# Optimization experiments

Hardware: AMD Instinct MI355X
Metric: run time of the kernel (lower is better)

The kernel has to match this reference:

```python
import jax, jax.numpy as jnp
import numpy as np

D_IN = 128
HID = 32
HEADS = 8
OUT = 16
N = 50000
E = 400000
NEG_SLOPE = 0.2


def setup_inputs() -> dict:
    key = jax.random.key(0)
    ks = jax.random.split(key, 12)
    s = lambda k, sh: jax.random.normal(k, sh, dtype=jnp.float32) * 0.05
    return {
        "x": jax.random.normal(ks[0], (N, D_IN), dtype=jnp.float32),
        "edge_index": jax.random.randint(ks[1], (2, E), 0, N, dtype=jnp.int64),
        # conv_1: GATv2, heads=8, concat=True
        "W1l": s(ks[2], (D_IN, HEADS * HID)),
        "W1r": s(ks[3], (D_IN, HEADS * HID)),
        "att1": s(ks[4], (HEADS, HID)),
        "b1": jnp.zeros((HEADS * HID,), dtype=jnp.float32),
        # conv_2: GATv2, heads=1, concat=False
        "W2l": s(ks[5], (HEADS * HID, HID)),
        "W2r": s(ks[6], (HEADS * HID, HID)),
        "att2": s(ks[7], (1, HID)),
        "b2": jnp.zeros((HID,), dtype=jnp.float32),
        # final linear
        "Wlin": s(ks[8], (HID, OUT)),
        "blin": jnp.zeros((OUT,), dtype=jnp.float32),
    }


def _gatv2(x, src, dst, Wl, Wr, att, bias, n_nodes):
    heads, ch = att.shape
    xl = (x @ Wl).reshape(n_nodes, heads, ch)   # source-side transform
    xr = (x @ Wr).reshape(n_nodes, heads, ch)   # target-side transform
    # per-edge GATv2 score: a^T leaky_relu(xl_i + xr_j)
    e = jax.nn.leaky_relu(xl[src] + xr[dst], NEG_SLOPE)        # [E,H,C]
    logits = jnp.einsum('ehc,hc->eh', e, att)                  # [E,H]
    # segment softmax grouped by destination node
    m = jax.ops.segment_max(logits, dst, num_segments=n_nodes)
    m = jnp.where(jnp.isfinite(m), m, 0.0)
    p = jnp.exp(logits - m[dst])
    denom = jax.ops.segment_sum(p, dst, num_segments=n_nodes)
    alpha = p / jnp.maximum(denom[dst], 1e-16)                 # [E,H]
    # scatter-sum aggregation of weighted source features
    out = jax.ops.segment_sum(alpha[:, :, None] * xl[src], dst, num_segments=n_nodes)
    return out + bias.reshape(1, heads, ch)                    # [N,H,C]


def reference(x, edge_index, W1l, W1r, att1, b1, W2l, W2r, att2, b2, Wlin, blin):
    n = x.shape[0]
    loops = jnp.arange(n, dtype=edge_index.dtype)
    ei = jnp.concatenate([edge_index, jnp.stack([loops, loops])], axis=1)  # add_self_loops=True
    src, dst = ei[0], ei[1]

    h = _gatv2(x, src, dst, W1l, W1r, att1, b1, n)   # [N,8,32]
    h = jax.nn.elu(h.reshape(n, -1))                  # concat=True; dropout=identity (eval)

    h = _gatv2(h, src, dst, W2l, W2r, att2, b2, n)   # [N,1,32]
    h = jax.nn.elu(h[:, 0, :])                        # concat=False, heads=1 -> mean == squeeze

    return h @ Wlin + blin                            # [N,16]
```

## Files before the change

kernel.cpp:

```cpp
#include <hip/hip_runtime.h>
#include <cstdint>
#include <cstddef>

#define N_NODES 50000
#define N_EDGES 400000
#define E_TOT   (N_EDGES + N_NODES)
#define D_INF   128
#define C1      256
#define HIDC    32
#define OUTC    16
#define NEG_SLOPE 0.2f
#define LOG2E   1.44269504088896340736f

#define SEG_CAP 64

#define SCAT_T  (N_EDGES / 4)
#define SLOOP_T ((N_NODES + 3) / 4)
#define SCATB   ((SCAT_T + SLOOP_T + 255) / 256)
#define UNITS16 (N_NODES / 16)
#define U16PAD  (UNITS16 + 1)
#define NU32    ((N_NODES + 31) / 32)
#define XPB     UNITS16
#define WPB     40
#define PREPB   (SCATB + XPB + WPB)
#define GBLK    ((2 * NU32 + 3) / 4)

typedef __bf16 bf16x8 __attribute__((ext_vector_type(8)));
typedef float  floatx4 __attribute__((ext_vector_type(4)));
typedef float  floatx2 __attribute__((ext_vector_type(2)));
typedef int    intx4  __attribute__((ext_vector_type(4)));
typedef unsigned int uintx4 __attribute__((ext_vector_type(4)));
typedef unsigned int uintx2 __attribute__((ext_vector_type(2)));
typedef unsigned short ushortx8 __attribute__((ext_vector_type(8)));
typedef unsigned short ushortx4 __attribute__((ext_vector_type(4)));

__device__ __forceinline__ unsigned short f2bf(float f) {
  unsigned int u = __builtin_bit_cast(unsigned int, f);
  u += 0x7FFFu + ((u >> 16) & 1u);
  return (unsigned short)(u >> 16);
}
__device__ __forceinline__ float bf2f(unsigned short u) {
  return __builtin_bit_cast(float, (unsigned int)u << 16);
}
__device__ __forceinline__ floatx2 bf2x2(unsigned int u) {
  floatx2 r;
  r.x = __builtin_bit_cast(float, u << 16);
  r.y = __builtin_bit_cast(float, u & 0xffff0000u);
  return r;
}

__global__ __launch_bounds__(256) void k_prep(
    const int* __restrict__ ei,
    const float* __restrict__ x, unsigned short* __restrict__ xpack,
    const float* __restrict__ W1l, const float* __restrict__ W1r,
    const float* __restrict__ W2l, const float* __restrict__ W2r,
    unsigned short* __restrict__ w1lp, unsigned short* __restrict__ w1rp,
    unsigned short* __restrict__ w2lp, unsigned short* __restrict__ w2rp,
    int* __restrict__ deg, int* __restrict__ esrc) {
  const int bid = blockIdx.x;
  const int tid = threadIdx.x;
  if (bid < SCATB) {
    __shared__ int sdet;
    if (tid == 0) sdet = 0;
    __syncthreads();
    if (tid < 64) atomicOr(&sdet, ei[2 * tid + 1]);
    __syncthreads();
    const bool f64 = (sdet == 0);

    const int t = bid * 256 + tid;
    int s4[4], d4[4];
    bool valid = false;
    if (t < SCAT_T) {
      valid = true;
      if (f64) {
        intx4 a = *reinterpret_cast<const intx4*>(ei + 8 * t);
        intx4 b = *reinterpret_cast<const intx4*>(ei + 8 * t + 4);
        intx4 c = *reinterpret_cast<const intx4*>(ei + 2 * N_EDGES + 8 * t);
        intx4 d = *reinterpret_cast<const intx4*>(ei + 2 * N_EDGES + 8 * t + 4);
        s4[0] = a.x; s4[1] = a.z; s4[2] = b.x; s4[3] = b.z;
        d4[0] = c.x; d4[1] = c.z; d4[2] = d.x; d4[3] = d.z;
      } else {
        intx4 a = *reinterpret_cast<const intx4*>(ei + 4 * t);
        intx4 c = *reinterpret_cast<const intx4*>(ei + N_EDGES + 4 * t);
        s4[0] = a.x; s4[1] = a.y; s4[2] = a.z; s4[3] = a.w;
        d4[0] = c.x; d4[1] = c.y; d4[2] = c.z; d4[3] = c.w;
      }
    } else if (t < SCAT_T + SLOOP_T) {
      valid = true;
      const int n0 = (t - SCAT_T) * 4;
      s4[0] = d4[0] = n0;     s4[1] = d4[1] = n0 + 1;
      s4[2] = d4[2] = n0 + 2; s4[3] = d4[3] = n0 + 3;
    }
    if (valid) {
      int pos[4];
#pragma unroll
      for (int j = 0; j < 4; ++j) {
        const bool ok = (unsigned)s4[j] < N_NODES && (unsigned)d4[j] < N_NODES;
        pos[j] = ok ? atomicAdd(&deg[d4[j]], 1) : SEG_CAP;
      }
#pragma unroll
      for (int j = 0; j < 4; ++j)
        if (pos[j] < SEG_CAP) esrc[((size_t)d4[j] << 6) + pos[j]] = s4[j];
    }
    return;
  }
  if (bid < SCATB + XPB) {
    const int u = bid - SCATB;
    const int kb = tid >> 6, lane = tid & 63;
    const int row = u * 16 + (lane & 15);
    const int k0 = kb * 32 + (lane >> 4) * 8;
    floatx4 a = *reinterpret_cast<const floatx4*>(x + (size_t)row * D_INF + k0);
    floatx4 b = *reinterpret_cast<const floatx4*>(x + (size_t)row * D_INF + k0 + 4);
    ushortx8 u8;
#pragma unroll
    for (int j = 0; j < 4; ++j) { u8[j] = f2bf(a[j]); u8[4 + j] = f2bf(b[j]); }
    *reinterpret_cast<ushortx8*>(xpack + ((size_t)(u * 4 + kb) * 64 + lane) * 8) = u8;
    return;
  }
  int f = (bid - SCATB - XPB) * 256 + tid;
  if (f < 8192) {
    const float* W = (f < 4096) ? W1l : W1r;
    unsigned short* P = (f < 4096) ? w1lp : w1rp;
    f &= 4095;
    const int nt = f >> 8, kb = (f >> 6) & 3, lane = f & 63;
    const int col = nt * 16 + (lane & 15);
    const int k0 = kb * 32 + (lane >> 4) * 8;
    ushortx8 u8;
#pragma unroll
    for (int j = 0; j < 8; ++j) u8[j] = f2bf(W[(size_t)(k0 + j) * C1 + col]);
    *reinterpret_cast<ushortx8*>(P + (size_t)f * 8) = u8;
  } else {
    f -= 8192;
    const float* W = (f < 1024) ? W2l : W2r;
    unsigned short* P = (f < 1024) ? w2lp : w2rp;
    f &= 1023;
    const int nt = f >> 9, kb = (f >> 6) & 7, lane = f & 63;
    const int col = nt * 16 + (lane & 15);
    const int k0 = kb * 32 + (lane >> 4) * 8;
    ushortx8 u8;
#pragma unroll
    for (int j = 0; j < 8; ++j) u8[j] = f2bf(W[(size_t)(k0 + j) * HIDC + col]);
    *reinterpret_cast<ushortx8*>(P + (size_t)f * 8) = u8;
  }
}

__device__ __forceinline__ bf16x8 ldfrag(const unsigned short* base, int lane) {
  uintx4 raw = *reinterpret_cast<const uintx4*>(base + (size_t)lane * 8);
  return __builtin_bit_cast(bf16x8, raw);
}

template <int KB, int NCOLS>
__device__ __forceinline__ void gemm_body32(
    int u, int lane, const unsigned short* __restrict__ Ap,
    const unsigned short* __restrict__ Bp, unsigned short* __restrict__ C) {
  const int lo = lane & 15;
  const int q  = lane >> 4;
  const int r0 = u * 32;
  const bool two = (r0 + 16) < N_NODES;

  bf16x8 af[2][KB];
#pragma unroll
  for (int rg = 0; rg < 2; ++rg)
#pragma unroll
    for (int kb = 0; kb < KB; ++kb)
      af[rg][kb] = ldfrag(Ap + ((size_t)(u * 2 + rg) * KB + kb) * 64 * 8, lane);

#pragma unroll 4
  for (int nt = 0; nt < NCOLS / 16; ++nt) {
    bf16x8 b[KB];
#pragma unroll
    for (int kb = 0; kb < KB; ++kb)
      b[kb] = ldfrag(Bp + ((size_t)nt * KB + kb) * 64 * 8, lane);
    floatx4 acc0 = {0.f, 0.f, 0.f, 0.f};
    floatx4 acc1 = {0.f, 0.f, 0.f, 0.f};
#pragma unroll
    for (int kb = 0; kb < KB; ++kb) {
      acc0 = __builtin_amdgcn_mfma_f32_16x16x32_bf16(af[0][kb], b[kb], acc0, 0, 0, 0);
      acc1 = __builtin_amdgcn_mfma_f32_16x16x32_bf16(af[1][kb], b[kb], acc1, 0, 0, 0);
    }
#pragma unroll
    for (int r = 0; r < 4; ++r) {
      C[(size_t)(r0 + q * 4 + r) * NCOLS + nt * 16 + lo] = f2bf(acc0[r]);
      if (two)
        C[(size_t)(r0 + 16 + q * 4 + r) * NCOLS + nt * 16 + lo] = f2bf(acc1[r]);
    }
  }
}

__global__ __launch_bounds__(256) void k_gemm1(
    const unsigned short* __restrict__ Ap,
    const unsigned short* __restrict__ B0, const unsigned short* __restrict__ B1,
    unsigned short* __restrict__ C0, unsigned short* __restrict__ C1_) {
  const int wave = threadIdx.x >> 6;
  const int lane = threadIdx.x & 63;
  const int unit = blockIdx.x * 4 + wave;
  if (unit >= 2 * NU32) return;
  const int o = (unit >= NU32) ? 1 : 0;
  gemm_body32<4, C1>(unit - o * NU32, lane, Ap, o ? B1 : B0, o ? C1_ : C0);
}

__global__ __launch_bounds__(256) void k_gemm2(
    const unsigned short* __restrict__ Ap,
    const unsigned short* __restrict__ B0, const unsigned short* __restrict__ B1,
    unsigned short* __restrict__ C0, unsigned short* __restrict__ C1_) {
  const int wave = threadIdx.x >> 6;
  const int lane = threadIdx.x & 63;
  const int unit = blockIdx.x * 4 + wave;
  if (unit >= 2 * NU32) return;
  const int o = (unit >= NU32) ? 1 : 0;
  gemm_body32<8, HIDC>(unit - o * NU32, lane, Ap, o ? B1 : B0, o ? C1_ : C0);
}

__global__ __launch_bounds__(256) void k_gat1(
    const unsigned short* __restrict__ xl1, const unsigned short* __restrict__ xr1,
    const float* __restrict__ att1, const float* __restrict__ b1,
    const int* __restrict__ deg, const int* __restrict__ esrc,
    unsigned short* __restrict__ h1pack) {
  const int wave = threadIdx.x >> 6;
  const int lane = threadIdx.x & 63;
  const int dst = blockIdx.x * 4 + wave;
  if (dst >= N_NODES) return;
  const int h = lane >> 5;
  const int w = lane & 31;
  const int cb = w * 8;

  floatx2 xr2v[4], att2v[4];
  {
    uintx4 r = *reinterpret_cast<const uintx4*>(xr1 + (size_t)dst * C1 + cb);
    floatx4 a0 = *reinterpret_cast<const floatx4*>(att1 + cb);
    floatx4 a1 = *reinterpret_cast<const floatx4*>(att1 + cb + 4);
#pragma unroll
    for (int j = 0; j < 4; ++j) xr2v[j] = bf2x2(r[j]);
    att2v[0] = floatx2{a0.x, a0.y} * LOG2E;
    att2v[1] = floatx2{a0.z, a0.w} * LOG2E;
    att2v[2] = floatx2{a1.x, a1.y} * LOG2E;
    att2v[3] = floatx2{a1.z, a1.w} * LOG2E;
  }

  const int n = min(deg[dst], SEG_CAP);
  const int* __restrict__ ep = esrc + ((size_t)dst << 6);

  float l = 0.f;
  floatx2 acc2[4] = {{0.f, 0.f}, {0.f, 0.f}, {0.f, 0.f}, {0.f, 0.f}};

  auto process = [&](uintx4 cur) {
    floatx2 xs2[4];
    floatx2 v2 = {0.f, 0.f};
#pragma unroll
    for (int j = 0; j < 4; ++j) {
      xs2[j] = bf2x2(cur[j]);
      floatx2 s2 = xs2[j] + xr2v[j];
      floatx2 e2 = __builtin_elementwise_max(s2, s2 * NEG_SLOPE);
      v2 = __builtin_elementwise_fma(e2, att2v[j], v2);
    }
    float v = v2.x + v2.y;
    v += __shfl_xor(v, 1);
    v += __shfl_xor(v, 2);
    v = __builtin_amdgcn_fmed3f(v, -100.f, 100.f);
    const float p = __builtin_amdgcn_exp2f(v);
    l += p;
    const floatx2 p2 = {p, p};
#pragma unroll
    for (int j = 0; j < 4; ++j)
      acc2[j] = __builtin_elementwise_fma(p2, xs2[j], acc2[j]);
  };

  uintx4 bufa = {0u, 0u, 0u, 0u}, bufb = {0u, 0u, 0u, 0u};
  if (h < n)
    bufa = *reinterpret_cast<const uintx4*>(xl1 + (size_t)ep[h] * C1 + cb);
  if (h + 2 < n)
    bufb = *reinterpret_cast<const uintx4*>(xl1 + (size_t)ep[h + 2] * C1 + cb);
  int i = h;
  while (i < n) {
    process(bufa);
    if (i + 4 < n)
      bufa = *reinterpret_cast<const uintx4*>(xl1 + (size_t)ep[i + 4] * C1 + cb);
    i += 2;
    if (i >= n) break;
    process(bufb);
    if (i + 4 < n)
      bufb = *reinterpret_cast<const uintx4*>(xl1 + (size_t)ep[i + 4] * C1 + cb);
    i += 2;
  }

  l += __shfl_xor(l, 32);
#pragma unroll
  for (int j = 0; j < 4; ++j) {
    acc2[j].x += __shfl_xor(acc2[j].x, 32);
    acc2[j].y += __shfl_xor(acc2[j].y, 32);
  }

  if (h == 0) {
    const float inv = 1.f / fmaxf(l, 1e-16f);
    ushortx8 ob;
#pragma unroll
    for (int j = 0; j < 4; ++j) {
      float z0 = acc2[j].x * inv + b1[cb + 2 * j];
      float z1 = acc2[j].y * inv + b1[cb + 2 * j + 1];
      z0 = z0 > 0.f ? z0 : (__expf(z0) - 1.f);
      z1 = z1 > 0.f ? z1 : (__expf(z1) - 1.f);
      ob[2 * j]     = f2bf(z0);
      ob[2 * j + 1] = f2bf(z1);
    }
    const size_t frag = ((size_t)(dst >> 4) * 8 + (cb >> 5)) * 64
                      + ((cb >> 3) & 3) * 16 + (dst & 15);
    *reinterpret_cast<ushortx8*>(h1pack + frag * 8) = ob;
  }
}

__global__ __launch_bounds__(256) void k_gat2(
    const unsigned short* __restrict__ xl2, const unsigned short* __restrict__ xr2,
    const float* __restrict__ att2, const float* __restrict__ b2,
    const float* __restrict__ Wlin, const float* __restrict__ blin,
    const int* __restrict__ deg, const int* __restrict__ esrc,
    float* __restrict__ out) {
  __shared__ float sh[4][32];
  const int wave = threadIdx.x >> 6;
  const int lane = threadIdx.x & 63;
  const int dst = blockIdx.x * 4 + wave;
  if (dst >= N_NODES) return;
  const int o8 = lane >> 3;
  const int w = lane & 7;
  const int cb = w * 4;

  floatx2 xr2v[2], att2v[2];
  {
    uintx2 r = *reinterpret_cast<const uintx2*>(xr2 + (size_t)dst * HIDC + cb);
    floatx4 a = *reinterpret_cast<const floatx4*>(att2 + cb);
    xr2v[0] = bf2x2(r[0]);
    xr2v[1] = bf2x2(r[1]);
    att2v[0] = floatx2{a.x, a.y} * LOG2E;
    att2v[1] = floatx2{a.z, a.w} * LOG2E;
  }

  const int n = min(deg[dst], SEG_CAP);
  const int* __restrict__ ep = esrc + ((size_t)dst << 6);

  float l = 0.f;
  floatx2 acc2[2] = {{0.f, 0.f}, {0.f, 0.f}};

  auto process = [&](uintx2 cur) {
    floatx2 xs2[2];
    floatx2 v2 = {0.f, 0.f};
#pragma unroll
    for (int j = 0; j < 2; ++j) {
      xs2[j] = bf2x2(cur[j]);
      floatx2 s2 = xs2[j] + xr2v[j];
      floatx2 e2 = __builtin_elementwise_max(s2, s2 * NEG_SLOPE);
      v2 = __builtin_elementwise_fma(e2, att2v[j], v2);
    }
    float v = v2.x + v2.y;
    v += __shfl_xor(v, 1);
    v += __shfl_xor(v, 2);
    v += __shfl_xor(v, 4);
    v = __builtin_amdgcn_fmed3f(v, -100.f, 100.f);
    const float p = __builtin_amdgcn_exp2f(v);
    l += p;
    const floatx2 p2 = {p, p};
#pragma unroll
    for (int j = 0; j < 2; ++j)
      acc2[j] = __builtin_elementwise_fma(p2, xs2[j], acc2[j]);
  };

  uintx2 bufa = {0u, 0u}, bufb = {0u, 0u};
  if (o8 < n)
    bufa = *reinterpret_cast<const uintx2*>(xl2 + (size_t)ep[o8] * HIDC + cb);
  if (o8 + 8 < n)
    bufb = *reinterpret_cast<const uintx2*>(xl2 + (size_t)ep[o8 + 8] * HIDC + cb);
  int i = o8;
  while (i < n) {
    process(bufa);
    if (i + 16 < n)
      bufa = *reinterpret_cast<const uintx2*>(xl2 + (size_t)ep[i + 16] * HIDC + cb);
    i += 8;
    if (i >= n) break;
    process(bufb);
    if (i + 16 < n)
      bufb = *reinterpret_cast<const uintx2*>(xl2 + (size_t)ep[i + 16] * HIDC + cb);
    i += 8;
  }

#pragma unroll
  for (int k = 8; k < 64; k <<= 1) {
    l += __shfl_xor(l, k);
#pragma unroll
    for (int j = 0; j < 2; ++j) {
      acc2[j].x += __shfl_xor(acc2[j].x, k);
      acc2[j].y += __shfl_xor(acc2[j].y, k);
    }
  }

  if (o8 == 0) {
    const float inv = 1.f / fmaxf(l, 1e-16f);
#pragma unroll
    for (int j = 0; j < 2; ++j) {
      float z0 = acc2[j].x * inv + b2[cb + 2 * j];
      float z1 = acc2[j].y * inv + b2[cb + 2 * j + 1];
      z0 = z0 > 0.f ? z0 : (__expf(z0) - 1.f);
      z1 = z1 > 0.f ? z1 : (__expf(z1) - 1.f);
      sh[wave][cb + 2 * j]     = z0;
      sh[wave][cb + 2 * j + 1] = z1;
    }
  }
  if (lane < OUTC) {
    float o = blin[lane];
#pragma unroll
    for (int k = 0; k < 32; ++k)
      o = fmaf(sh[wave][k], Wlin[k * OUTC + lane], o);
    out[(size_t)dst * OUTC + lane] = o;
  }
}

static inline int cdiv(int a, int b) { return (a + b - 1) / b; }

extern "C" void kernel_launch(void* const* d_in, const int* in_sizes, int n_in,
                              void* d_out, int out_size, void* d_ws, size_t ws_size,
                              hipStream_t stream) {
  const float* x    = (const float*)d_in[0];
  const int*   ei   = (const int*)d_in[1];
  const float* W1l  = (const float*)d_in[2];
  const float* W1r  = (const float*)d_in[3];
  const float* att1 = (const float*)d_in[4];
  const float* b1   = (const float*)d_in[5];
  const float* W2l  = (const float*)d_in[6];
  const float* W2r  = (const float*)d_in[7];
  const float* att2 = (const float*)d_in[8];
  const float* b2   = (const float*)d_in[9];
  const float* Wlin = (const float*)d_in[10];
  const float* blin = (const float*)d_in[11];
  float* out = (float*)d_out;

  char* w = (char*)d_ws;
  auto alloc = [&](size_t bytes) -> char* {
    char* p = w;
    w += (bytes + 255) & ~(size_t)255;
    return p;
  };
  char* regionA = alloc((size_t)N_NODES * C1 * 2);
  unsigned short* xl1 = (unsigned short*)regionA;
  unsigned short* xl2 = (unsigned short*)regionA;
  unsigned short* xr2 = (unsigned short*)(regionA + (size_t)N_NODES * HIDC * 2 + 256);
  unsigned short* xr1 = (unsigned short*)alloc((size_t)N_NODES * C1 * 2);
  unsigned short* xpack  = (unsigned short*)alloc((size_t)U16PAD * 4 * 64 * 8 * 2);
  unsigned short* h1pack = (unsigned short*)alloc((size_t)U16PAD * 8 * 64 * 8 * 2);
  unsigned short* w1lp = (unsigned short*)alloc((size_t)4096 * 8 * 2);
  unsigned short* w1rp = (unsigned short*)alloc((size_t)4096 * 8 * 2);
  unsigned short* w2lp = (unsigned short*)alloc((size_t)1024 * 8 * 2);
  unsigned short* w2rp = (unsigned short*)alloc((size_t)1024 * 8 * 2);
  int* deg    = (int*)alloc((size_t)N_NODES * 4);
  int* esrc   = (int*)alloc((size_t)N_NODES * SEG_CAP * 4);

  hipMemsetAsync(deg, 0, (size_t)N_NODES * 4, stream);

  k_prep<<<PREPB, 256, 0, stream>>>(ei, x, xpack, W1l, W1r, W2l, W2r,
                                    w1lp, w1rp, w2lp, w2rp, deg, esrc);

  k_gemm1<<<GBLK, 256, 0, stream>>>(xpack, w1lp, w1rp, xl1, xr1);

  k_gat1<<<cdiv(N_NODES, 4), 256, 0, stream>>>(xl1, xr1, att1, b1,
                                               deg, esrc, h1pack);

  k_gemm2<<<GBLK, 256, 0, stream>>>(h1pack, w2lp, w2rp, xl2, xr2);

  k_gat2<<<cdiv(N_NODES, 4), 256, 0, stream>>>(xl2, xr2, att2, b2, Wlin, blin,
                                               deg, esrc, out);
}
```

Before: 223.7 us.

## Move edge scatter into gemm1 launch and deepen gather prefetch in gat1

Moves the edge bucketing (degree atomics and the esrc scatter) out of the prep kernel and appends it as extra blocks to the layer-1 GEMM launch, so the atomic-heavy scatter can overlap with MFMA work. The gat1 neighbor gather goes from double to triple buffering to keep more loads in flight, and both GAT kernels switch to 32-bit byte-offset addressing from a common base pointer. The xr1 load relies on pointer arithmetic between two separate allocations, and the triple buffer adds register pressure.

```diff
diff --git a/kernel.cpp b/kernel.cpp
--- a/kernel.cpp
+++ b/kernel.cpp
@@ -22,7 +22,7 @@
 #define NU32    ((N_NODES + 31) / 32)
 #define XPB     UNITS16
 #define WPB     40
-#define PREPB   (SCATB + XPB + WPB)
+#define PREPB   (XPB + WPB)
 #define GBLK    ((2 * NU32 + 3) / 4)
 
 typedef __bf16 bf16x8 __attribute__((ext_vector_type(8)));
@@ -50,62 +50,15 @@
 }
 
 __global__ __launch_bounds__(256) void k_prep(
-    const int* __restrict__ ei,
     const float* __restrict__ x, unsigned short* __restrict__ xpack,
     const float* __restrict__ W1l, const float* __restrict__ W1r,
     const float* __restrict__ W2l, const float* __restrict__ W2r,
     unsigned short* __restrict__ w1lp, unsigned short* __restrict__ w1rp,
-    unsigned short* __restrict__ w2lp, unsigned short* __restrict__ w2rp,
-    int* __restrict__ deg, int* __restrict__ esrc) {
+    unsigned short* __restrict__ w2lp, unsigned short* __restrict__ w2rp) {
   const int bid = blockIdx.x;
   const int tid = threadIdx.x;
-  if (bid < SCATB) {
-    __shared__ int sdet;
-    if (tid == 0) sdet = 0;
-    __syncthreads();
-    if (tid < 64) atomicOr(&sdet, ei[2 * tid + 1]);
-    __syncthreads();
-    const bool f64 = (sdet == 0);
-
-    const int t = bid * 256 + tid;
-    int s4[4], d4[4];
-    bool valid = false;
-    if (t < SCAT_T) {
-      valid = true;
-      if (f64) {
-        intx4 a = *reinterpret_cast<const intx4*>(ei + 8 * t);
-        intx4 b = *reinterpret_cast<const intx4*>(ei + 8 * t + 4);
-        intx4 c = *reinterpret_cast<const intx4*>(ei + 2 * N_EDGES + 8 * t);
-        intx4 d = *reinterpret_cast<const intx4*>(ei + 2 * N_EDGES + 8 * t + 4);
-        s4[0] = a.x; s4[1] = a.z; s4[2] = b.x; s4[3] = b.z;
-        d4[0] = c.x; d4[1] = c.z; d4[2] = d.x; d4[3] = d.z;
-      } else {
-        intx4 a = *reinterpret_cast<const intx4*>(ei + 4 * t);
-        intx4 c = *reinterpret_cast<const intx4*>(ei + N_EDGES + 4 * t);
-        s4[0] = a.x; s4[1] = a.y; s4[2] = a.z; s4[3] = a.w;
-        d4[0] = c.x; d4[1] = c.y; d4[2] = c.z; d4[3] = c.w;
-      }
-    } else if (t < SCAT_T + SLOOP_T) {
-      valid = true;
-      const int n0 = (t - SCAT_T) * 4;
-      s4[0] = d4[0] = n0;     s4[1] = d4[1] = n0 + 1;
-      s4[2] = d4[2] = n0 + 2; s4[3] = d4[3] = n0 + 3;
-    }
-    if (valid) {
-      int pos[4];
-#pragma unroll
-      for (int j = 0; j < 4; ++j) {
-        const bool ok = (unsigned)s4[j] < N_NODES && (unsigned)d4[j] < N_NODES;
-        pos[j] = ok ? atomicAdd(&deg[d4[j]], 1) : SEG_CAP;
-      }
-#pragma unroll
-      for (int j = 0; j < 4; ++j)
-        if (pos[j] < SEG_CAP) esrc[((size_t)d4[j] << 6) + pos[j]] = s4[j];
-    }
-    return;
-  }
-  if (bid < SCATB + XPB) {
-    const int u = bid - SCATB;
+  if (bid < XPB) {
+    const int u = bid;
     const int kb = tid >> 6, lane = tid & 63;
     const int row = u * 16 + (lane & 15);
     const int k0 = kb * 32 + (lane >> 4) * 8;
@@ -117,7 +70,7 @@
     *reinterpret_cast<ushortx8*>(xpack + ((size_t)(u * 4 + kb) * 64 + lane) * 8) = u8;
     return;
   }
-  int f = (bid - SCATB - XPB) * 256 + tid;
+  int f = (bid - XPB) * 256 + tid;
   if (f < 8192) {
     const float* W = (f < 4096) ? W1l : W1r;
     unsigned short* P = (f < 4096) ? w1lp : w1rp;
@@ -190,13 +143,61 @@
 __global__ __launch_bounds__(256) void k_gemm1(
     const unsigned short* __restrict__ Ap,
     const unsigned short* __restrict__ B0, const unsigned short* __restrict__ B1,
-    unsigned short* __restrict__ C0, unsigned short* __restrict__ C1_) {
-  const int wave = threadIdx.x >> 6;
-  const int lane = threadIdx.x & 63;
-  const int unit = blockIdx.x * 4 + wave;
-  if (unit >= 2 * NU32) return;
-  const int o = (unit >= NU32) ? 1 : 0;
-  gemm_body32<4, C1>(unit - o * NU32, lane, Ap, o ? B1 : B0, o ? C1_ : C0);
+    unsigned short* __restrict__ C0, unsigned short* __restrict__ C1_,
+    const int* __restrict__ ei, int* __restrict__ deg, int* __restrict__ esrc) {
+  const int tid = threadIdx.x;
+  if (blockIdx.x < GBLK) {
+    const int wave = tid >> 6;
+    const int lane = tid & 63;
+    const int unit = blockIdx.x * 4 + wave;
+    if (unit >= 2 * NU32) return;
+    const int o = (unit >= NU32) ? 1 : 0;
+    gemm_body32<4, C1>(unit - o * NU32, lane, Ap, o ? B1 : B0, o ? C1_ : C0);
+    return;
+  }
+  const int bid = blockIdx.x - GBLK;
+  __shared__ int sdet;
+  if (tid == 0) sdet = 0;
+  __syncthreads();
+  if (tid < 64) atomicOr(&sdet, ei[2 * tid + 1]);
+  __syncthreads();
+  const bool f64 = (sdet == 0);
+
+  const int t = bid * 256 + tid;
+  int s4[4], d4[4];
+  bool valid = false;
+  if (t < SCAT_T) {
+    valid = true;
+    if (f64) {
+      intx4 a = *reinterpret_cast<const intx4*>(ei + 8 * t);
+      intx4 b = *reinterpret_cast<const intx4*>(ei + 8 * t + 4);
+      intx4 c = *reinterpret_cast<const intx4*>(ei + 2 * N_EDGES + 8 * t);
+      intx4 d = *reinterpret_cast<const intx4*>(ei + 2 * N_EDGES + 8 * t + 4);
+      s4[0] = a.x; s4[1] = a.z; s4[2] = b.x; s4[3] = b.z;
+      d4[0] = c.x; d4[1] = c.z; d4[2] = d.x; d4[3] = d.z;
+    } else {
+      intx4 a = *reinterpret_cast<const intx4*>(ei + 4 * t);
+      intx4 c = *reinterpret_cast<const intx4*>(ei + N_EDGES + 4 * t);
+      s4[0] = a.x; s4[1] = a.y; s4[2] = a.z; s4[3] = a.w;
+      d4[0] = c.x; d4[1] = c.y; d4[2] = c.z; d4[3] = c.w;
+    }
+  } else if (t < SCAT_T + SLOOP_T) {
+    valid = true;
+    const int n0 = (t - SCAT_T) * 4;
+    s4[0] = d4[0] = n0;     s4[1] = d4[1] = n0 + 1;
+    s4[2] = d4[2] = n0 + 2; s4[3] = d4[3] = n0 + 3;
+  }
+  if (valid) {
+    int pos[4];
+#pragma unroll
+    for (int j = 0; j < 4; ++j) {
+      const bool ok = (unsigned)s4[j] < N_NODES && (unsigned)d4[j] < N_NODES;
+      pos[j] = ok ? atomicAdd(&deg[d4[j]], 1) : SEG_CAP;
+    }
+#pragma unroll
+    for (int j = 0; j < 4; ++j)
+      if (pos[j] < SEG_CAP) esrc[((size_t)d4[j] << 6) + pos[j]] = s4[j];
+  }
 }
 
 __global__ __launch_bounds__(256) void k_gemm2(
@@ -223,10 +224,13 @@
   const int h = lane >> 5;
   const int w = lane & 31;
   const int cb = w * 8;
+  const unsigned cb2 = (unsigned)cb * 2u;
+  const char* __restrict__ xbase = (const char*)xl1;
 
   floatx2 xr2v[4], att2v[4];
   {
-    uintx4 r = *reinterpret_cast<const uintx4*>(xr1 + (size_t)dst * C1 + cb);
+    uintx4 r = *reinterpret_cast<const uintx4*>(
+        xbase + (((unsigned)dst << 9) + cb2) + ((const char*)xr1 - (const char*)xl1));
     floatx4 a0 = *reinterpret_cast<const floatx4*>(att1 + cb);
     floatx4 a1 = *reinterpret_cast<const floatx4*>(att1 + cb + 4);
 #pragma unroll
@@ -243,6 +247,10 @@
   float l = 0.f;
   floatx2 acc2[4] = {{0.f, 0.f}, {0.f, 0.f}, {0.f, 0.f}, {0.f, 0.f}};
 
+  auto L = [&](int s) {
+    const unsigned off = ((unsigned)s << 9) + cb2;
+    return *reinterpret_cast<const uintx4*>(xbase + off);
+  };
   auto process = [&](uintx4 cur) {
     floatx2 xs2[4];
     floatx2 v2 = {0.f, 0.f};
@@ -265,21 +273,22 @@
       acc2[j] = __builtin_elementwise_fma(p2, xs2[j], acc2[j]);
   };
 
-  uintx4 bufa = {0u, 0u, 0u, 0u}, bufb = {0u, 0u, 0u, 0u};
-  if (h < n)
-    bufa = *reinterpret_cast<const uintx4*>(xl1 + (size_t)ep[h] * C1 + cb);
-  if (h + 2 < n)
-    bufb = *reinterpret_cast<const uintx4*>(xl1 + (size_t)ep[h + 2] * C1 + cb);
+  uintx4 bufa = {0u,0u,0u,0u}, bufb = {0u,0u,0u,0u}, bufc = {0u,0u,0u,0u};
+  if (h     < n) bufa = L(ep[h]);
+  if (h + 2 < n) bufb = L(ep[h + 2]);
+  if (h + 4 < n) bufc = L(ep[h + 4]);
   int i = h;
   while (i < n) {
     process(bufa);
-    if (i + 4 < n)
-      bufa = *reinterpret_cast<const uintx4*>(xl1 + (size_t)ep[i + 4] * C1 + cb);
+    if (i + 6 < n) bufa = L(ep[i + 6]);
     i += 2;
     if (i >= n) break;
     process(bufb);
-    if (i + 4 < n)
-      bufb = *reinterpret_cast<const uintx4*>(xl1 + (size_t)ep[i + 4] * C1 + cb);
+    if (i + 6 < n) bufb = L(ep[i + 6]);
+    i += 2;
+    if (i >= n) break;
+    process(bufc);
+    if (i + 6 < n) bufc = L(ep[i + 6]);
     i += 2;
   }
 
@@ -322,6 +331,8 @@
   const int o8 = lane >> 3;
   const int w = lane & 7;
   const int cb = w * 4;
+  const unsigned cb2 = (unsigned)cb * 2u;
+  const char* __restrict__ xbase = (const char*)xl2;
 
   floatx2 xr2v[2], att2v[2];
   {
@@ -339,6 +350,10 @@
   float l = 0.f;
   floatx2 acc2[2] = {{0.f, 0.f}, {0.f, 0.f}};
 
+  auto L = [&](int s) {
+    const unsigned off = ((unsigned)s << 6) + cb2;
+    return *reinterpret_cast<const uintx2*>(xbase + off);
+  };
   auto process = [&](uintx2 cur) {
     floatx2 xs2[2];
     floatx2 v2 = {0.f, 0.f};
@@ -363,20 +378,16 @@
   };
 
   uintx2 bufa = {0u, 0u}, bufb = {0u, 0u};
-  if (o8 < n)
-    bufa = *reinterpret_cast<const uintx2*>(xl2 + (size_t)ep[o8] * HIDC + cb);
-  if (o8 + 8 < n)
-    bufb = *reinterpret_cast<const uintx2*>(xl2 + (size_t)ep[o8 + 8] * HIDC + cb);
+  if (o8 < n)     bufa = L(ep[o8]);
+  if (o8 + 8 < n) bufb = L(ep[o8 + 8]);
   int i = o8;
   while (i < n) {
     process(bufa);
-    if (i + 16 < n)
-      bufa = *reinterpret_cast<const uintx2*>(xl2 + (size_t)ep[i + 16] * HIDC + cb);
+    if (i + 16 < n) bufa = L(ep[i + 16]);
     i += 8;
     if (i >= n) break;
     process(bufb);
-    if (i + 16 < n)
-      bufb = *reinterpret_cast<const uintx2*>(xl2 + (size_t)ep[i + 16] * HIDC + cb);
+    if (i + 16 < n) bufb = L(ep[i + 16]);
     i += 8;
   }
 
@@ -452,10 +463,11 @@
 
   hipMemsetAsync(deg, 0, (size_t)N_NODES * 4, stream);
 
-  k_prep<<<PREPB, 256, 0, stream>>>(ei, x, xpack, W1l, W1r, W2l, W2r,
-                                    w1lp, w1rp, w2lp, w2rp, deg, esrc);
-
-  k_gemm1<<<GBLK, 256, 0, stream>>>(xpack, w1lp, w1rp, xl1, xr1);
+  k_prep<<<PREPB, 256, 0, stream>>>(x, xpack, W1l, W1r, W2l, W2r,
+                                    w1lp, w1rp, w2lp, w2rp);
+
+  k_gemm1<<<GBLK + SCATB, 256, 0, stream>>>(xpack, w1lp, w1rp, xl1, xr1,
+                                            ei, deg, esrc);
 
   k_gat1<<<cdiv(N_NODES, 4), 256, 0, stream>>>(xl1, xr1, att1, b1,
                                                deg, esrc, h1pack);
```

New measurement: 231.8 us. 1.04x slower.
